# Kernel tuning notes

Measured on AMD Instinct MI355X. Metric: run time of the kernel, lower is better.

Reference implementation:

```python
import jax, jax.numpy as jnp
import numpy as np

N_NODES = 100000
N_EDGES = 500000
D = 128        # node feat dim == output dim
DT = 128       # time encoding dim
DE = 128       # edge feat dim
B = 300
K = 2
NN = 20
N_HEADS = 2
N_LAYERS = 2


def setup_inputs() -> dict:
    key = jax.random.key(0)
    ks = jax.random.split(key, 20)
    s = 0.05
    inp = {
        "node_features": jax.random.normal(ks[0], (N_NODES, D), jnp.float32) * s,
        "edge_features": jax.random.normal(ks[1], (N_EDGES, DE), jnp.float32) * s,
        "time_w": jax.random.normal(ks[2], (1, DT), jnp.float32),
        "time_b": jax.random.normal(ks[3], (DT,), jnp.float32),
        "Wq": jax.random.normal(ks[4], (N_LAYERS, D + DT, D), jnp.float32) * s,
        "Wk": jax.random.normal(ks[5], (N_LAYERS, D + DT + DE, D), jnp.float32) * s,
        "Wv": jax.random.normal(ks[6], (N_LAYERS, D + DT + DE, D), jnp.float32) * s,
        "Wo": jax.random.normal(ks[7], (N_LAYERS, D, D), jnp.float32) * s,
        "fc1": jax.random.normal(ks[8], (N_LAYERS, 2 * D, D), jnp.float32) * s,
        "fc2": jax.random.normal(ks[9], (N_LAYERS, D, D), jnp.float32) * s,
        "source_nodes": jax.random.randint(ks[10], (B,), 0, N_NODES),
        "timestamps": jax.random.uniform(ks[11], (B,), jnp.float32, 500.0, 1000.0),
        "neigh2": jax.random.randint(ks[12], (B, K, NN), 0, N_NODES),
        "eidx2": jax.random.randint(ks[13], (B, K, NN), 0, N_EDGES),
        "etimes2": jax.random.uniform(ks[14], (B, K, NN), jnp.float32, 0.0, 500.0),
        "neigh1": jax.random.randint(ks[15], (B * K * NN, K, NN), 0, N_NODES),
        "eidx1": jax.random.randint(ks[16], (B * K * NN, K, NN), 0, N_EDGES),
        "etimes1": jax.random.uniform(ks[17], (B * K * NN, K, NN), jnp.float32, 0.0, 500.0),
    }
    return inp


def reference(node_features, edge_features, time_w, time_b,
              Wq, Wk, Wv, Wo, fc1, fc2,
              source_nodes, timestamps,
              neigh2, eidx2, etimes2,
              neigh1, eidx1, etimes1):
    d = node_features.shape[1]
    dh = d // N_HEADS

    def time_enc(t):  # t: [...] -> [..., DT], TGAT-style cosine time encoding
        return jnp.cos(t[..., None] * time_w[0] + time_b)

    def hop_agg(layer, src_nodes, ts, neigh, eidx, etimes, neigh_emb):
        # neigh/eidx/etimes: [b, K, NN]; neigh_emb: [b, K, NN, d]
        b = src_nodes.shape[0]
        kn = K * NN
        src = node_features[src_nodes]                         # [b, d]
        src_t = time_enc(jnp.zeros((b,), ts.dtype))            # [b, DT]
        deltas = ts[:, None, None] - etimes                    # [b, K, NN]
        et = time_enc(deltas.reshape(b, kn))                   # [b, kn, DT]
        ef = edge_features[eidx].reshape(b, kn, -1)            # [b, kn, DE]
        ne = neigh_emb.reshape(b, kn, -1)                      # [b, kn, d]
        mask = neigh.reshape(b, kn) == 0                       # padded neighbors

        q = jnp.concatenate([src, src_t], axis=-1) @ Wq[layer]            # [b, d]
        kv_in = jnp.concatenate([ne, et, ef], axis=-1)                    # [b, kn, d+DT+DE]
        kk = kv_in @ Wk[layer]                                            # [b, kn, d]
        vv = kv_in @ Wv[layer]

        qh = q.reshape(b, N_HEADS, dh)
        kh = kk.reshape(b, kn, N_HEADS, dh)
        vh = vv.reshape(b, kn, N_HEADS, dh)
        scores = jnp.einsum('bhd,bnhd->bhn', qh, kh) / jnp.sqrt(jnp.float32(dh))
        scores = jnp.where(mask[:, None, :], jnp.float32(-1e9), scores)
        attn = jax.nn.softmax(scores, axis=-1)                            # [b, h, kn]
        out = jnp.einsum('bhn,bnhd->bhd', attn, vh).reshape(b, d) @ Wo[layer]
        merged = jnp.concatenate([out, src], axis=-1)                     # [b, 2d]
        return jax.nn.relu(merged @ fc1[layer]) @ fc2[layer]              # [b, d]

    # --- recursion unrolled (n_layers = 2) ---
    # level 0: raw node features of 2-hop neighbors
    b1 = neigh2.shape[0] * K * NN
    emb0 = node_features[neigh1.reshape(-1)].reshape(b1, K, NN, d)
    ts1 = jnp.repeat(timestamps, K * NN)
    # level 1 aggregation (attention_models[0])
    emb1 = hop_agg(0, neigh2.reshape(-1), ts1, neigh1, eidx1, etimes1, emb0)
    # level 2 aggregation (attention_models[1])
    emb2 = hop_agg(1, source_nodes, timestamps,
                   neigh2, eidx2, etimes2,
                   emb1.reshape(source_nodes.shape[0], K, NN, d))
    return emb2
```

## Files before the change

kernel.cpp:

```cpp
#include <hip/hip_runtime.h>
#include <cstdint>

typedef _Float16 half_t;
typedef _Float16 half8  __attribute__((ext_vector_type(8)));
typedef _Float16 half4_t __attribute__((ext_vector_type(4)));
typedef _Float16 h2f    __attribute__((ext_vector_type(2)));
typedef float    floatx4 __attribute__((ext_vector_type(4)));

#define KNN 40
#define KVPAD 124

#define WS_NF16    0ull
#define WS_EMB16   25600000ull
#define WS_WKVT    28672000ull
#define WS_WQ4     29065216ull
#define WS_W1A4    29196288ull
#define WS_W1B4    29327360ull
#define WS_W24     29458432ull
#define WS_QBIAS   29589504ull
#define WS_WOFTMP  29590528ull
#define WS_ZERO    29721600ull
#define WS_EF16    29721856ull
#define WS_TOTAL_FULL (WS_EF16 + 128000000ull)

__device__ __forceinline__ void ld16(const void* g, void* l) {
  __builtin_amdgcn_global_load_lds(
      (const __attribute__((address_space(1))) unsigned int*)(uintptr_t)g,
      (__attribute__((address_space(3))) unsigned int*)(uintptr_t)l, 16, 0, 0);
}

__device__ __forceinline__ float dot4(half4_t a, half4_t b, float s) {
  s = __builtin_amdgcn_fdot2((h2f){a[0], a[1]}, (h2f){b[0], b[1]}, s, false);
  s = __builtin_amdgcn_fdot2((h2f){a[2], a[3]}, (h2f){b[2], b[3]}, s, false);
  return s;
}

__global__ __launch_bounds__(256) void cvt_kernel(
    const float* __restrict__ src, half_t* __restrict__ dst, int n8) {
  int stride = gridDim.x * 256;
  for (int i = blockIdx.x * 256 + threadIdx.x; i < n8; i += stride) {
    float4 a = *((const float4*)src + 2 * (size_t)i);
    float4 b = *((const float4*)src + 2 * (size_t)i + 1);
    half8 h;
    h[0] = (half_t)a.x; h[1] = (half_t)a.y; h[2] = (half_t)a.z; h[3] = (half_t)a.w;
    h[4] = (half_t)b.x; h[5] = (half_t)b.y; h[6] = (half_t)b.z; h[7] = (half_t)b.w;
    *((half8*)dst + i) = h;
  }
}

#define PK_DECODE(t) int l = (t) >> 14; int u = (t) & 16383; \
  int d4 = u >> 9; int v = u & 511; int j = v >> 2; int e = v & 3;

__global__ __launch_bounds__(256) void precompute_w(
    const float* __restrict__ Wq, const float* __restrict__ Wk,
    const float* __restrict__ Wv, const float* __restrict__ Wo,
    const float* __restrict__ fc1, const float* __restrict__ fc2,
    const float* __restrict__ time_b,
    half_t* __restrict__ WkvT, float* __restrict__ qbias,
    float* __restrict__ woftmp, half_t* __restrict__ Wq4,
    half_t* __restrict__ W1b4, half_t* __restrict__ W24,
    half_t* __restrict__ zrow)
{
  int blk = blockIdx.x, tid = threadIdx.x;
  if (blk < 768) {
    int t = blk * 256 + tid;
    int l = t / 98304;
    int r = t - l * 98304;
    int n = r / 384;
    int k = r - n * 384;
    float vv = (n < 128) ? Wk[l * 49152 + k * 128 + n]
                         : Wv[l * 49152 + k * 128 + (n - 128)];
    WkvT[t] = (half_t)vv;
  } else if (blk == 768) {
    if (tid < 128) zrow[tid] = (half_t)0.f;
    int l = tid >> 7, j = tid & 127;
    float s = 0.f;
    for (int d = 0; d < 128; ++d)
      s += cosf(time_b[d]) * Wq[l * 32768 + (128 + d) * 128 + j];
    qbias[l * 128 + j] = s;
  } else if (blk < 897) {
    int t = (blk - 769) * 256 + tid;
    int l = t >> 14;
    int r = t & 16383;
    int dd = r >> 7, j = r & 127;
    float s = 0.f;
    for (int m = 0; m < 128; ++m)
      s += Wo[l * 16384 + dd * 128 + m] * fc1[l * 32768 + m * 128 + j];
    woftmp[t] = s;
  } else if (blk < 1025) {
    int t = (blk - 897) * 256 + tid;
    PK_DECODE(t);
    Wq4[t] = (half_t)Wq[l * 32768 + (4 * d4 + e) * 128 + j];
  } else if (blk < 1153) {
    int t = (blk - 1025) * 256 + tid;
    PK_DECODE(t);
    W1b4[t] = (half_t)fc1[l * 32768 + (128 + 4 * d4 + e) * 128 + j];
  } else {
    int t = (blk - 1153) * 256 + tid;
    PK_DECODE(t);
    W24[t] = (half_t)fc2[l * 16384 + (4 * d4 + e) * 128 + j];
  }
}

__global__ __launch_bounds__(256) void precompute_w2(
    const float* __restrict__ woftmp, half_t* __restrict__ W1a4) {
  int t = blockIdx.x * 256 + threadIdx.x;
  PK_DECODE(t);
  W1a4[t] = (half_t)woftmp[l * 16384 + (4 * d4 + e) * 128 + j];
}

template <bool EF16, bool L1DIR>
__global__ __launch_bounds__(512, 4) void hop_kernel(
    const float*  __restrict__ nf,
    const half_t* __restrict__ ne16,
    const half_t* __restrict__ ef16,
    const float*  __restrict__ ef32,
    const int*    __restrict__ src_idx,
    const float*  __restrict__ tsv,
    const int*    __restrict__ neigh,
    const int*    __restrict__ eidx,
    const float*  __restrict__ etimes,
    const float*  __restrict__ tw,
    const float*  __restrict__ tb,
    const half_t* __restrict__ Wq4_l,
    const float*  __restrict__ qbias_l,
    const half_t* __restrict__ WkvT_l,
    const half_t* __restrict__ W1a4_l,
    const half_t* __restrict__ W1b4_l,
    const half_t* __restrict__ W24_l,
    const half_t* __restrict__ zrow,
    half_t* __restrict__ out16,
    float*  __restrict__ out32)
{
  __shared__ __align__(16) char smem[71360];
  half_t* BTs  = (half_t*)(smem + 32768);
  half_t* kvT  = (half_t*)(smem + 32768);
  float*  tw_s = (float*)(smem + 65536);
  float*  tb_s = (float*)(smem + 66048);
  float*  qs   = (float*)(smem + 66560);
  half_t* s16  = (half_t*)(smem + 68096);
  half_t* aO16 = (half_t*)(smem + 68864);
  half_t* h116 = (half_t*)(smem + 69632);
  float*  scs  = (float*)(smem + 70400);

  const int tid = threadIdx.x;
  const int bbase = blockIdx.x * 3;
  const int lane = tid & 63, wv = tid >> 6;
  const int l15 = lane & 15, q4 = lane >> 4;
  const int wm = (wv & 1) * 64, wn = (wv >> 1) * 64;

  if (tid < 128) { tw_s[tid] = tw[tid]; tb_s[tid] = tb[tid]; }
  if (tid < 96) {
    int g = tid >> 5, d4 = tid & 31;
    float4 v4 = *(const float4*)(nf + (size_t)src_idx[bbase + g] * 128 + d4 * 4);
    half4_t h;
    h[0] = (half_t)v4.x; h[1] = (half_t)v4.y; h[2] = (half_t)v4.z; h[3] = (half_t)v4.w;
    *(half4_t*)(s16 + g * 128 + d4 * 4) = h;
  }

  const int r = wv * 16 + l15;
  const bool valid = (r < 120);
  float dval = 0.f;
  const half_t* pNE = zrow + q4 * 8;
  const half_t* pEF = zrow + q4 * 8;
  if (valid) {
    int g = r / 40, n = r - g * 40;
    int bg = bbase + g;
    int rowidx = bg * KNN + n;
    dval = tsv[L1DIR ? bg : (bg / 40)] - etimes[rowidx];
    pNE = (L1DIR ? ne16 + (size_t)rowidx * 128
                 : ne16 + (size_t)neigh[rowidx] * 128) + q4 * 8;
    if (EF16) pEF = ef16 + (size_t)eidx[rowidx] * 128 + q4 * 8;
  }
  const float* gbe32 = nullptr;
  const int rr = tid >> 2, pp = tid & 3;
  if (!EF16 && rr < 120) {
    int g2 = rr / 40, n2 = rr - g2 * 40;
    gbe32 = ef32 + (size_t)eidx[(bbase + g2) * KNN + n2] * 128 + pp * 16;
  }

  const half_t* bBase = WkvT_l + (size_t)(2 * wv * 16 + l15) * 384 + q4 * 8;

  floatx4 acc[4][4];
  #pragma unroll
  for (int mi = 0; mi < 4; ++mi)
    #pragma unroll
    for (int ni = 0; ni < 4; ++ni) acc[mi][ni] = (floatx4){0.f, 0.f, 0.f, 0.f};

  auto issueA = [&](const half_t* p, int koff, char* buf) {
    ld16(p + koff,      buf + wv * 2048);
    ld16(p + koff + 32, buf + wv * 2048 + 1024);
  };
  auto issueB = [&](int kc) {
    const half_t* bp = bBase + kc * 64;
    ld16(bp,          (char*)BTs + wv * 4096);
    ld16(bp + 32,     (char*)BTs + wv * 4096 + 1024);
    ld16(bp + 6144,   (char*)BTs + wv * 4096 + 2048);
    ld16(bp + 6176,   (char*)BTs + wv * 4096 + 3072);
  };
  auto cosA = [&](int koff, char* buf) {
    #pragma unroll
    for (int i = 0; i < 2; ++i) {
      int c = i * 4 + q4;
      half8 h;
      #pragma unroll
      for (int j = 0; j < 8; ++j) {
        float ang = __builtin_fmaf(dval, tw_s[koff + c * 8 + j], tb_s[koff + c * 8 + j]);
        h[j] = valid ? (half_t)__cosf(ang) : (half_t)0.f;
      }
      *(half8*)(buf + wv * 2048 + i * 1024 + lane * 16) = h;
    }
  };
  auto efA32 = [&](int koff, char* buf) {
    half8 h0 = {}, h1 = {};
    if (rr < 120) {
      const float* gb = gbe32 + koff;
      float4 v0 = ((const float4*)gb)[0];
      float4 v1 = ((const float4*)gb)[1];
      float4 v2 = ((const float4*)gb)[2];
      float4 v3 = ((const float4*)gb)[3];
      h0[0] = (half_t)v0.x; h0[1] = (half_t)v0.y; h0[2] = (half_t)v0.z; h0[3] = (half_t)v0.w;
      h0[4] = (half_t)v1.x; h0[5] = (half_t)v1.y; h0[6] = (half_t)v1.z; h0[7] = (half_t)v1.w;
      h1[0] = (half_t)v2.x; h1[1] = (half_t)v2.y; h1[2] = (half_t)v2.z; h1[3] = (half_t)v2.w;
      h1[4] = (half_t)v3.x; h1[5] = (half_t)v3.y; h1[6] = (half_t)v3.z; h1[7] = (half_t)v3.w;
    }
    half_t* Ad = (half_t*)buf + (((rr >> 4) * 8) + 2 * pp) * 128 + (rr & 15) * 8;
    *(half8*)Ad = h0;
    *(half8*)(Ad + 128) = h1;
  };
  auto mfma_step = [&](const char* abuf) {
    #pragma unroll
    for (int ks = 0; ks < 2; ++ks) {
      int c = ks * 4 + q4;
      half8 a[4];
      #pragma unroll
      for (int mi = 0; mi < 4; ++mi)
        a[mi] = *(const half8*)((const half_t*)abuf + (((wm >> 4) + mi) * 8 + c) * 128 + l15 * 8);
      #pragma unroll
      for (int ni = 0; ni < 4; ++ni) {
        half8 bfr = *(const half8*)(BTs + (((wn >> 4) + ni) * 8 + c) * 128 + l15 * 8);
        #pragma unroll
        for (int mi = 0; mi < 4; ++mi)
          acc[mi][ni] = __builtin_amdgcn_mfma_f32_16x16x32_f16(a[mi], bfr, acc[mi][ni], 0, 0, 0);
      }
    }
  };

  issueA(pNE, 0, smem);
  issueA(pNE, 64, smem + 16384);
  {
    const char* sw = (const char*)Wq4_l + wv * 4096 + lane * 16;
    char* dw = (char*)BTs + wv * 4096;
    ld16(sw, dw); ld16(sw + 1024, dw + 1024);
    ld16(sw + 2048, dw + 2048); ld16(sw + 3072, dw + 3072);
  }
  __syncthreads();

  if (tid < 384) {
    int gq = tid >> 7, jj = tid & 127;
    float s = qbias_l[jj];
    #pragma unroll 8
    for (int d4 = 0; d4 < 32; ++d4) {
      half4_t w = *(const half4_t*)(BTs + (d4 * 128 + jj) * 4);
      half4_t a = *(const half4_t*)(s16 + gq * 128 + d4 * 4);
      s = dot4(w, a, s);
    }
    qs[gq * 128 + jj] = s;
  }
  __syncthreads();

  issueB(0); __syncthreads(); mfma_step(smem);          __syncthreads();
  cosA(0, smem);
  issueB(1); __syncthreads(); mfma_step(smem + 16384);  __syncthreads();
  cosA(64, smem + 16384);
  issueB(2); __syncthreads(); mfma_step(smem);          __syncthreads();
  if (EF16) issueA(pEF, 0, smem); else efA32(0, smem);
  issueB(3); __syncthreads(); mfma_step(smem + 16384);  __syncthreads();
  if (EF16) issueA(pEF, 64, smem + 16384); else efA32(64, smem + 16384);
  issueB(4); __syncthreads(); mfma_step(smem);          __syncthreads();
  issueB(5); __syncthreads(); mfma_step(smem + 16384);  __syncthreads();

  {
    const char* sw = (const char*)W1a4_l + wv * 4096 + lane * 16;
    char* dw = smem + wv * 4096;
    ld16(sw, dw); ld16(sw + 1024, dw + 1024);
    ld16(sw + 2048, dw + 2048); ld16(sw + 3072, dw + 3072);
  }

  if (wv < 4) {
    #pragma unroll
    for (int mi = 0; mi < 4; ++mi) {
      int row0 = wm + mi * 16 + q4 * 4;
      if (row0 < 120) {
        #pragma unroll
        for (int ni = 0; ni < 4; ++ni) {
          int col = wn + ni * 16 + l15;
          half4_t h;
          h[0] = (half_t)acc[mi][ni][0]; h[1] = (half_t)acc[mi][ni][1];
          h[2] = (half_t)acc[mi][ni][2]; h[3] = (half_t)acc[mi][ni][3];
          *(half4_t*)(kvT + col * KVPAD + row0) = h;
        }
      }
    }
  }
  __syncthreads();

  if (tid < 240) {
    int g = tid / 80;
    int rem = tid - g * 80;
    int h = rem / 40;
    int n = rem - h * 40;
    bool masked = (neigh[(bbase + g) * KNN + n] == 0);
    const float* qrow = qs + g * 128 + h * 64;
    int row = g * 40 + n;
    float s = 0.f;
    #pragma unroll 8
    for (int d = 0; d < 64; ++d)
      s += qrow[d] * (float)kvT[(h * 64 + d) * KVPAD + row];
    scs[tid] = masked ? -1e9f : s * 0.125f;
  }
  __syncthreads();

  if (wv < 6) {
    float v = (lane < 40) ? scs[wv * 40 + lane] : -1e30f;
    float m = v;
    #pragma unroll
    for (int o = 32; o; o >>= 1) m = fmaxf(m, __shfl_xor(m, o));
    float e = (lane < 40) ? __expf(v - m) : 0.f;
    float ssum = e;
    #pragma unroll
    for (int o = 32; o; o >>= 1) ssum += __shfl_xor(ssum, o);
    if (lane < 40) scs[wv * 40 + lane] = e / ssum;
  }
  if (wv >= 4) {
    #pragma unroll
    for (int mi = 0; mi < 4; ++mi) {
      int row0 = wm + mi * 16 + q4 * 4;
      if (row0 < 120) {
        #pragma unroll
        for (int ni = 0; ni < 4; ++ni) {
          int col = wn - 128 + ni * 16 + l15;
          half4_t h;
          h[0] = (half_t)acc[mi][ni][0]; h[1] = (half_t)acc[mi][ni][1];
          h[2] = (half_t)acc[mi][ni][2]; h[3] = (half_t)acc[mi][ni][3];
          *(half4_t*)(kvT + col * KVPAD + row0) = h;
        }
      }
    }
  }
  __syncthreads();

  if (tid < 384) {
    int g = tid >> 7, dcol = tid & 127, h = dcol >> 6;
    const float* attn = scs + (g * 2 + h) * 40;
    const half_t* vcol = kvT + dcol * KVPAD + g * 40;
    float s = 0.f;
    #pragma unroll 8
    for (int n = 0; n < 40; ++n) s += attn[n] * (float)vcol[n];
    aO16[g * 128 + dcol] = (half_t)s;
  }
  __syncthreads();

  {
    const char* sw = (const char*)W1b4_l + wv * 4096 + lane * 16;
    char* dw = (char*)BTs + wv * 4096;
    ld16(sw, dw); ld16(sw + 1024, dw + 1024);
    ld16(sw + 2048, dw + 2048); ld16(sw + 3072, dw + 3072);
  }
  float p1 = 0.f;
  if (tid < 384) {
    int g = tid >> 7, jj = tid & 127;
    #pragma unroll 8
    for (int d4 = 0; d4 < 32; ++d4) {
      half4_t w = *(const half4_t*)((const half_t*)smem + (d4 * 128 + jj) * 4);
      half4_t a = *(const half4_t*)(aO16 + g * 128 + d4 * 4);
      p1 = dot4(w, a, p1);
    }
  }
  __syncthreads();

  {
    const char* sw = (const char*)W24_l + wv * 4096 + lane * 16;
    char* dw = smem + wv * 4096;
    ld16(sw, dw); ld16(sw + 1024, dw + 1024);
    ld16(sw + 2048, dw + 2048); ld16(sw + 3072, dw + 3072);
  }
  if (tid < 384) {
    int g = tid >> 7, jj = tid & 127;
    float p2 = p1;
    #pragma unroll 8
    for (int d4 = 0; d4 < 32; ++d4) {
      half4_t w = *(const half4_t*)(BTs + (d4 * 128 + jj) * 4);
      half4_t a = *(const half4_t*)(s16 + g * 128 + d4 * 4);
      p2 = dot4(w, a, p2);
    }
    h116[g * 128 + jj] = (half_t)fmaxf(p2, 0.f);
  }
  __syncthreads();

  if (tid < 384) {
    int g = tid >> 7, ii = tid & 127;
    float s = 0.f;
    #pragma unroll 8
    for (int j4 = 0; j4 < 32; ++j4) {
      half4_t w = *(const half4_t*)((const half_t*)smem + (j4 * 128 + ii) * 4);
      half4_t a = *(const half4_t*)(h116 + g * 128 + j4 * 4);
      s = dot4(w, a, s);
    }
    if (L1DIR) out32[(size_t)(bbase + g) * 128 + ii] = s;
    else       out16[(size_t)(bbase + g) * 128 + ii] = (half_t)s;
  }
}

extern "C" void kernel_launch(void* const* d_in, const int* in_sizes, int n_in,
                              void* d_out, int out_size, void* d_ws, size_t ws_size,
                              hipStream_t stream) {
  const float* nf      = (const float*)d_in[0];
  const float* ef      = (const float*)d_in[1];
  const float* tw      = (const float*)d_in[2];
  const float* tb      = (const float*)d_in[3];
  const float* Wq      = (const float*)d_in[4];
  const float* Wk      = (const float*)d_in[5];
  const float* Wv      = (const float*)d_in[6];
  const float* Wo      = (const float*)d_in[7];
  const float* fc1     = (const float*)d_in[8];
  const float* fc2     = (const float*)d_in[9];
  const int*   srcn    = (const int*)d_in[10];
  const float* ts      = (const float*)d_in[11];
  const int*   neigh2  = (const int*)d_in[12];
  const int*   eidx2   = (const int*)d_in[13];
  const float* etimes2 = (const float*)d_in[14];
  const int*   neigh1  = (const int*)d_in[15];
  const int*   eidx1   = (const int*)d_in[16];
  const float* etimes1 = (const float*)d_in[17];

  char* ws = (char*)d_ws;
  half_t* nf16   = (half_t*)(ws + WS_NF16);
  half_t* emb116 = (half_t*)(ws + WS_EMB16);
  half_t* WkvT16 = (half_t*)(ws + WS_WKVT);
  half_t* Wq4    = (half_t*)(ws + WS_WQ4);
  half_t* W1a4   = (half_t*)(ws + WS_W1A4);
  half_t* W1b4   = (half_t*)(ws + WS_W1B4);
  half_t* W24    = (half_t*)(ws + WS_W24);
  float*  qbias  = (float*)(ws + WS_QBIAS);
  float*  woftmp = (float*)(ws + WS_WOFTMP);
  half_t* zrow   = (half_t*)(ws + WS_ZERO);
  half_t* ef16   = (half_t*)(ws + WS_EF16);

  bool full = (ws_size >= WS_TOTAL_FULL);

  cvt_kernel<<<dim3(2048), dim3(256), 0, stream>>>(nf, nf16, 1600000);
  if (full)
    cvt_kernel<<<dim3(4096), dim3(256), 0, stream>>>(ef, ef16, 8000000);
  precompute_w<<<dim3(1281), dim3(256), 0, stream>>>(
      Wq, Wk, Wv, Wo, fc1, fc2, tb, WkvT16, qbias, woftmp, Wq4, W1b4, W24, zrow);
  precompute_w2<<<dim3(128), dim3(256), 0, stream>>>(woftmp, W1a4);

  if (full) {
    hop_kernel<true, false><<<dim3(4000), dim3(512), 0, stream>>>(
        nf, nf16, ef16, ef, neigh2, ts, neigh1, eidx1, etimes1, tw, tb,
        Wq4, qbias, WkvT16, W1a4, W1b4, W24, zrow, emb116, nullptr);
    hop_kernel<true, true><<<dim3(100), dim3(512), 0, stream>>>(
        nf, emb116, ef16, ef, srcn, ts, neigh2, eidx2, etimes2, tw, tb,
        Wq4 + 16384, qbias + 128, WkvT16 + 98304, W1a4 + 16384, W1b4 + 16384,
        W24 + 16384, zrow, emb116, (float*)d_out);
  } else {
    hop_kernel<false, false><<<dim3(4000), dim3(512), 0, stream>>>(
        nf, nf16, ef16, ef, neigh2, ts, neigh1, eidx1, etimes1, tw, tb,
        Wq4, qbias, WkvT16, W1a4, W1b4, W24, zrow, emb116, nullptr);
    hop_kernel<false, true><<<dim3(100), dim3(512), 0, stream>>>(
        nf, emb116, ef16, ef, srcn, ts, neigh2, eidx2, etimes2, tw, tb,
        Wq4 + 16384, qbias + 128, WkvT16 + 98304, W1a4 + 16384, W1b4 + 16384,
        W24 + 16384, zrow, emb116, (float*)d_out);
  }
}
```

Measured before the change: 733.8 us.

## Software-pipeline K/V GEMM with finer k-steps and explicit vmcnt barriers

Reworks the fused K/V projection main loop into 12 smaller 32-wide k-steps. A 4-deep A buffer and a double-buffered B buffer are filled by async global-to-LDS loads issued ahead of use. Full __syncthreads are replaced by hand-placed s_waitcnt vmcnt/lgkmcnt counts plus s_barrier, so loads stay in flight across barriers. The Q projection moves after the GEMM and reads Wq directly from global, and the neighbor mask is prefetched early. Correctness now depends on the hand-computed wait counts matching the number of outstanding loads per path (EF16 vs fp32 edge features), which is fragile.

```diff
diff --git a/kernel.cpp b/kernel.cpp
--- a/kernel.cpp
+++ b/kernel.cpp
@@ -158,6 +158,12 @@
     *(half4_t*)(s16 + g * 128 + d4 * 4) = h;
   }
 
+  int neighval = 1;
+  if (tid < 240) {
+    int g = tid / 80, rem = tid - g * 80, n = rem % 40;
+    neighval = neigh[(bbase + g) * KNN + n];
+  }
+
   const int r = wv * 16 + l15;
   const bool valid = (r < 120);
   float dval = 0.f;
@@ -176,7 +182,7 @@
   const int rr = tid >> 2, pp = tid & 3;
   if (!EF16 && rr < 120) {
     int g2 = rr / 40, n2 = rr - g2 * 40;
-    gbe32 = ef32 + (size_t)eidx[(bbase + g2) * KNN + n2] * 128 + pp * 16;
+    gbe32 = ef32 + (size_t)eidx[(bbase + g2) * KNN + n2] * 128 + pp * 8;
   }
 
   const half_t* bBase = WkvT_l + (size_t)(2 * wv * 16 + l15) * 384 + q4 * 8;
@@ -187,105 +193,92 @@
     #pragma unroll
     for (int ni = 0; ni < 4; ++ni) acc[mi][ni] = (floatx4){0.f, 0.f, 0.f, 0.f};
 
-  auto issueA = [&](const half_t* p, int koff, char* buf) {
-    ld16(p + koff,      buf + wv * 2048);
-    ld16(p + koff + 32, buf + wv * 2048 + 1024);
-  };
-  auto issueB = [&](int kc) {
-    const half_t* bp = bBase + kc * 64;
-    ld16(bp,          (char*)BTs + wv * 4096);
-    ld16(bp + 32,     (char*)BTs + wv * 4096 + 1024);
-    ld16(bp + 6144,   (char*)BTs + wv * 4096 + 2048);
-    ld16(bp + 6176,   (char*)BTs + wv * 4096 + 3072);
-  };
-  auto cosA = [&](int koff, char* buf) {
-    #pragma unroll
-    for (int i = 0; i < 2; ++i) {
-      int c = i * 4 + q4;
-      half8 h;
-      #pragma unroll
-      for (int j = 0; j < 8; ++j) {
-        float ang = __builtin_fmaf(dval, tw_s[koff + c * 8 + j], tb_s[koff + c * 8 + j]);
-        h[j] = valid ? (half_t)__cosf(ang) : (half_t)0.f;
-      }
-      *(half8*)(buf + wv * 2048 + i * 1024 + lane * 16) = h;
-    }
-  };
-  auto efA32 = [&](int koff, char* buf) {
-    half8 h0 = {}, h1 = {};
+  auto issB = [&](int s, char* bb) {
+    int kc = (s < 4) ? s : (s < 8 ? s + 4 : s - 4);
+    const half_t* bp = bBase + kc * 32;
+    ld16(bp,        bb + wv * 2048);
+    ld16(bp + 6144, bb + wv * 2048 + 1024);
+  };
+  auto issA = [&](int s, char* ab) {
+    const half_t* p = (s < 4) ? pNE + s * 32 : pEF + (s - 4) * 32;
+    ld16(p, ab + wv * 1024);
+  };
+  auto cosA = [&](int s, char* ab) {
+    int cb = (s - 8) * 32 + q4 * 8;
+    half8 h;
+    #pragma unroll
+    for (int j = 0; j < 8; ++j) {
+      float ang = __builtin_fmaf(dval, tw_s[cb + j], tb_s[cb + j]);
+      h[j] = valid ? (half_t)__cosf(ang) : (half_t)0.f;
+    }
+    *(half8*)(ab + wv * 1024 + lane * 16) = h;
+  };
+  auto efA32 = [&](int s, char* ab) {
+    half8 h = {};
     if (rr < 120) {
-      const float* gb = gbe32 + koff;
+      const float* gb = gbe32 + (s - 4) * 32;
       float4 v0 = ((const float4*)gb)[0];
       float4 v1 = ((const float4*)gb)[1];
-      float4 v2 = ((const float4*)gb)[2];
-      float4 v3 = ((const float4*)gb)[3];
-      h0[0] = (half_t)v0.x; h0[1] = (half_t)v0.y; h0[2] = (half_t)v0.z; h0[3] = (half_t)v0.w;
-      h0[4] = (half_t)v1.x; h0[5] = (half_t)v1.y; h0[6] = (half_t)v1.z; h0[7] = (half_t)v1.w;
-      h1[0] = (half_t)v2.x; h1[1] = (half_t)v2.y; h1[2] = (half_t)v2.z; h1[3] = (half_t)v2.w;
-      h1[4] = (half_t)v3.x; h1[5] = (half_t)v3.y; h1[6] = (half_t)v3.z; h1[7] = (half_t)v3.w;
-    }
-    half_t* Ad = (half_t*)buf + (((rr >> 4) * 8) + 2 * pp) * 128 + (rr & 15) * 8;
-    *(half8*)Ad = h0;
-    *(half8*)(Ad + 128) = h1;
-  };
-  auto mfma_step = [&](const char* abuf) {
-    #pragma unroll
-    for (int ks = 0; ks < 2; ++ks) {
-      int c = ks * 4 + q4;
-      half8 a[4];
+      h[0] = (half_t)v0.x; h[1] = (half_t)v0.y; h[2] = (half_t)v0.z; h[3] = (half_t)v0.w;
+      h[4] = (half_t)v1.x; h[5] = (half_t)v1.y; h[6] = (half_t)v1.z; h[7] = (half_t)v1.w;
+    }
+    *(half8*)(ab + (rr >> 4) * 1024 + pp * 256 + (rr & 15) * 16) = h;
+  };
+  auto mfma_step = [&](const char* ab, const char* bb) {
+    const half_t* A  = (const half_t*)ab;
+    const half_t* Bp = (const half_t*)bb;
+    half8 a[4];
+    #pragma unroll
+    for (int mi = 0; mi < 4; ++mi)
+      a[mi] = *(const half8*)(A + ((wv & 1) * 4 + mi) * 512 + q4 * 128 + l15 * 8);
+    #pragma unroll
+    for (int ni = 0; ni < 4; ++ni) {
+      half8 bfr = *(const half8*)(Bp + (((wn >> 4) + ni) * 512) + q4 * 128 + l15 * 8);
       #pragma unroll
       for (int mi = 0; mi < 4; ++mi)
-        a[mi] = *(const half8*)((const half_t*)abuf + (((wm >> 4) + mi) * 8 + c) * 128 + l15 * 8);
-      #pragma unroll
-      for (int ni = 0; ni < 4; ++ni) {
-        half8 bfr = *(const half8*)(BTs + (((wn >> 4) + ni) * 8 + c) * 128 + l15 * 8);
-        #pragma unroll
-        for (int mi = 0; mi < 4; ++mi)
-          acc[mi][ni] = __builtin_amdgcn_mfma_f32_16x16x32_f16(a[mi], bfr, acc[mi][ni], 0, 0, 0);
-      }
-    }
-  };
-
-  issueA(pNE, 0, smem);
-  issueA(pNE, 64, smem + 16384);
-  {
-    const char* sw = (const char*)Wq4_l + wv * 4096 + lane * 16;
-    char* dw = (char*)BTs + wv * 4096;
+        acc[mi][ni] = __builtin_amdgcn_mfma_f32_16x16x32_f16(a[mi], bfr, acc[mi][ni], 0, 0, 0);
+    }
+  };
+  auto stageW = [&](const half_t* wsrc, char* dst) {
+    const char* sw = (const char*)wsrc + wv * 4096 + lane * 16;
+    char* dw = dst + wv * 4096;
     ld16(sw, dw); ld16(sw + 1024, dw + 1024);
     ld16(sw + 2048, dw + 2048); ld16(sw + 3072, dw + 3072);
-  }
-  __syncthreads();
-
-  if (tid < 384) {
-    int gq = tid >> 7, jj = tid & 127;
-    float s = qbias_l[jj];
-    #pragma unroll 8
-    for (int d4 = 0; d4 < 32; ++d4) {
-      half4_t w = *(const half4_t*)(BTs + (d4 * 128 + jj) * 4);
-      half4_t a = *(const half4_t*)(s16 + gq * 128 + d4 * 4);
-      s = dot4(w, a, s);
-    }
-    qs[gq * 128 + jj] = s;
-  }
-  __syncthreads();
-
-  issueB(0); __syncthreads(); mfma_step(smem);          __syncthreads();
-  cosA(0, smem);
-  issueB(1); __syncthreads(); mfma_step(smem + 16384);  __syncthreads();
-  cosA(64, smem + 16384);
-  issueB(2); __syncthreads(); mfma_step(smem);          __syncthreads();
-  if (EF16) issueA(pEF, 0, smem); else efA32(0, smem);
-  issueB(3); __syncthreads(); mfma_step(smem + 16384);  __syncthreads();
-  if (EF16) issueA(pEF, 64, smem + 16384); else efA32(64, smem + 16384);
-  issueB(4); __syncthreads(); mfma_step(smem);          __syncthreads();
-  issueB(5); __syncthreads(); mfma_step(smem + 16384);  __syncthreads();
-
-  {
-    const char* sw = (const char*)W1a4_l + wv * 4096 + lane * 16;
-    char* dw = smem + wv * 4096;
-    ld16(sw, dw); ld16(sw + 1024, dw + 1024);
-    ld16(sw + 2048, dw + 2048); ld16(sw + 3072, dw + 3072);
-  }
+  };
+
+#define AB(i) (smem + (i) * 8192)
+#define BB(i) (smem + 32768 + (i) * 16384)
+#define FENCE asm volatile("" ::: "memory")
+
+  FENCE;
+  issB(0, BB(0)); issB(1, BB(1));
+  issA(0, AB(0)); issA(1, AB(1)); issA(2, AB(2)); issA(3, AB(3));
+  asm volatile("s_waitcnt lgkmcnt(0)" ::: "memory");
+  __builtin_amdgcn_s_barrier(); FENCE;
+
+#define HSTEP(s, WE, WF, ...)                                                   \
+  asm volatile("s_waitcnt vmcnt(%0) lgkmcnt(0)" :: "i"(EF16 ? (WE) : (WF))      \
+               : "memory");                                                     \
+  __builtin_amdgcn_s_barrier(); FENCE;                                          \
+  mfma_step(AB((s) & 3), BB((s) & 1));                                          \
+  FENCE; __builtin_amdgcn_s_barrier(); FENCE;                                   \
+  __VA_ARGS__
+
+  HSTEP(0, 3, 3, issB(2, BB(0)); if constexpr (EF16) issA(4, AB(0)); else efA32(4, AB(0));)
+  HSTEP(1, 5, 4, issB(3, BB(1)); if constexpr (EF16) issA(5, AB(1)); else efA32(5, AB(1));)
+  HSTEP(2, 7, 5, issB(4, BB(0)); if constexpr (EF16) issA(6, AB(2)); else efA32(6, AB(2));)
+  HSTEP(3, 9, 6, issB(5, BB(1)); if constexpr (EF16) issA(7, AB(3)); else efA32(7, AB(3));)
+  HSTEP(4, 4, 2, issB(6, BB(0)); cosA(8, AB(0));)
+  HSTEP(5, 3, 2, issB(7, BB(1)); cosA(9, AB(1));)
+  HSTEP(6, 2, 2, issB(8, BB(0)); cosA(10, AB(2));)
+  HSTEP(7, 2, 2, issB(9, BB(1)); cosA(11, AB(3));)
+  HSTEP(8, 2, 2, issB(10, BB(0));)
+  HSTEP(9, 2, 2, issB(11, BB(1));)
+  HSTEP(10, 2, 2, )
+  HSTEP(11, 0, 0, )
+#undef HSTEP
+
+  stageW(W1a4_l, smem);
 
   if (wv < 4) {
     #pragma unroll
@@ -303,23 +296,36 @@
       }
     }
   }
-  __syncthreads();
+
+  if (tid < 384) {
+    int gq = tid >> 7, jj = tid & 127;
+    float s = qbias_l[jj];
+    #pragma unroll 8
+    for (int d4 = 0; d4 < 32; ++d4) {
+      half4_t w = *(const half4_t*)(Wq4_l + (d4 * 128 + jj) * 4);
+      half4_t a = *(const half4_t*)(s16 + gq * 128 + d4 * 4);
+      s = dot4(w, a, s);
+    }
+    qs[gq * 128 + jj] = s;
+  }
+  asm volatile("s_waitcnt lgkmcnt(0)" ::: "memory");
+  __builtin_amdgcn_s_barrier(); FENCE;
 
   if (tid < 240) {
     int g = tid / 80;
     int rem = tid - g * 80;
-    int h = rem / 40;
-    int n = rem - h * 40;
-    bool masked = (neigh[(bbase + g) * KNN + n] == 0);
-    const float* qrow = qs + g * 128 + h * 64;
+    int hh = rem / 40;
+    int n = rem - hh * 40;
+    const float* qrow = qs + g * 128 + hh * 64;
     int row = g * 40 + n;
     float s = 0.f;
     #pragma unroll 8
     for (int d = 0; d < 64; ++d)
-      s += qrow[d] * (float)kvT[(h * 64 + d) * KVPAD + row];
-    scs[tid] = masked ? -1e9f : s * 0.125f;
-  }
-  __syncthreads();
+      s += qrow[d] * (float)kvT[(hh * 64 + d) * KVPAD + row];
+    scs[tid] = (neighval == 0) ? -1e9f : s * 0.125f;
+  }
+  asm volatile("s_waitcnt lgkmcnt(0)" ::: "memory");
+  __builtin_amdgcn_s_barrier(); FENCE;
 
   if (wv < 6) {
     float v = (lane < 40) ? scs[wv * 40 + lane] : -1e30f;
@@ -348,25 +354,25 @@
       }
     }
   }
-  __syncthreads();
+  asm volatile("s_waitcnt lgkmcnt(0)" ::: "memory");
+  __builtin_amdgcn_s_barrier(); FENCE;
 
   if (tid < 384) {
-    int g = tid >> 7, dcol = tid & 127, h = dcol >> 6;
-    const float* attn = scs + (g * 2 + h) * 40;
+    int g = tid >> 7, dcol = tid & 127, hh = dcol >> 6;
+    const float* attn = scs + (g * 2 + hh) * 40;
     const half_t* vcol = kvT + dcol * KVPAD + g * 40;
     float s = 0.f;
     #pragma unroll 8
     for (int n = 0; n < 40; ++n) s += attn[n] * (float)vcol[n];
     aO16[g * 128 + dcol] = (half_t)s;
   }
-  __syncthreads();
-
-  {
-    const char* sw = (const char*)W1b4_l + wv * 4096 + lane * 16;
-    char* dw = (char*)BTs + wv * 4096;
-    ld16(sw, dw); ld16(sw + 1024, dw + 1024);
-    ld16(sw + 2048, dw + 2048); ld16(sw + 3072, dw + 3072);
-  }
+  asm volatile("s_waitcnt lgkmcnt(0)" ::: "memory");
+  __builtin_amdgcn_s_barrier(); FENCE;
+
+  stageW(W1b4_l, (char*)BTs);
+  asm volatile("s_waitcnt vmcnt(4)" ::: "memory");
+  __builtin_amdgcn_s_barrier(); FENCE;
+
   float p1 = 0.f;
   if (tid < 384) {
     int g = tid >> 7, jj = tid & 127;
@@ -377,14 +383,11 @@
       p1 = dot4(w, a, p1);
     }
   }
-  __syncthreads();
-
-  {
-    const char* sw = (const char*)W24_l + wv * 4096 + lane * 16;
-    char* dw = smem + wv * 4096;
-    ld16(sw, dw); ld16(sw + 1024, dw + 1024);
-    ld16(sw + 2048, dw + 2048); ld16(sw + 3072, dw + 3072);
-  }
+  FENCE; __builtin_amdgcn_s_barrier(); FENCE;
+
+  stageW(W24_l, smem);
+  asm volatile("s_waitcnt vmcnt(4)" ::: "memory");
+  __builtin_amdgcn_s_barrier(); FENCE;
   if (tid < 384) {
     int g = tid >> 7, jj = tid & 127;
     float p2 = p1;
@@ -396,7 +399,8 @@
     }
     h116[g * 128 + jj] = (half_t)fmaxf(p2, 0.f);
   }
-  __syncthreads();
+  asm volatile("s_waitcnt vmcnt(0) lgkmcnt(0)" ::: "memory");
+  __builtin_amdgcn_s_barrier(); FENCE;
 
   if (tid < 384) {
     int g = tid >> 7, ii = tid & 127;
@@ -410,6 +414,9 @@
     if (L1DIR) out32[(size_t)(bbase + g) * 128 + ii] = s;
     else       out16[(size_t)(bbase + g) * 128 + ii] = (half_t)s;
   }
+#undef AB
+#undef BB
+#undef FENCE
 }
 
 extern "C" void kernel_launch(void* const* d_in, const int* in_sizes, int n_in,
```

After: 706.4 us. 3.7% less time.
